# Kernel tuning notes

Measured on AMD Instinct MI355X. Metric: run time of the kernel, lower is better.

The kernel has to match this reference:

```python
import jax, jax.numpy as jnp
import numpy as np

GRID_MIN, GRID_MAX, GRID_SIZE = -4.0, 4.0, 12
BANDWIDTH = (GRID_MAX - GRID_MIN) / max(GRID_SIZE - 1, 1)  # 8/11


def setup_inputs() -> dict:
    key = jax.random.key(0)
    k1, k2, k3, k4 = jax.random.split(key, 4)
    B, I, O, G = 16384, 512, 512, GRID_SIZE
    x = jax.random.normal(k1, (B, I), dtype=jnp.float32)
    coeff = jax.random.normal(k2, (I, O, G), dtype=jnp.float32) * 0.05
    base_w = jax.random.normal(k3, (O, I), dtype=jnp.float32) * (1.0 / np.sqrt(I))
    base_b = jax.random.normal(k4, (O,), dtype=jnp.float32) * 0.01
    centers = jnp.linspace(GRID_MIN, GRID_MAX, G, dtype=jnp.float32)
    return {"x": x, "coeff": coeff, "base_w": base_w, "base_b": base_b, "centers": centers}


def reference(x, coeff, base_w, base_b, centers):
    # RBF basis: [B, I, G]
    diff = (x[..., None] - centers) / jnp.float32(BANDWIDTH)
    basis = jnp.exp(-0.5 * diff * diff)
    # spline contraction over in_dim and grid: [B, O]
    spline = jnp.einsum('big,iog->bo', basis, coeff)
    # residual base linear (torch Linear: x @ W^T + b)
    return spline + x @ base_w.T + base_b
```

## Files before the change

### kernel.cpp

```cpp
#include <hip/hip_runtime.h>
#include <hip/hip_bf16.h>


#define N_DIM 512
#define I_DIM 512
#define KTOT  6656
#define NSTEP 208

typedef short short8 __attribute__((ext_vector_type(8)));
typedef float f32x16 __attribute__((ext_vector_type(16)));
typedef unsigned int u32x4 __attribute__((ext_vector_type(4)));

#define CVTPK(dst, lo, hi) \
  asm("v_cvt_pk_bf16_f32 %0, %1, %2" : "=v"(dst) : "v"(lo), "v"(hi))

__device__ __forceinline__ unsigned short f2bf(float f) {
  union { float f; unsigned int u; } c; c.f = f;
  unsigned int r = (c.u + 0x7FFFu + ((c.u >> 16) & 1)) >> 16;
  return (unsigned short)r;
}

__global__ __launch_bounds__(256) void prep_w(const float* __restrict__ coeff,
                                              const float* __restrict__ base_w,
                                              unsigned short* __restrict__ Wb2) {
  int t = blockIdx.x * 256 + threadIdx.x;
  int e0 = (t & 1) * 4;
  int go = t >> 1;
  int o  = go & 511;
  int g  = go >> 9;
  int k4 = g * 8 + e0;
  int ic = k4 / 416;
  int rem = k4 - ic * 416;
  int slot = rem >> 5;
  int ii = rem & 31;
  int i = ic * 32 + ii;
  float v0, v1, v2, v3;
  if (slot == 0) {
    const float4 bw = *(const float4*)(base_w + (size_t)o * I_DIM + i);
    v0 = bw.x; v1 = bw.y; v2 = bw.z; v3 = bw.w;
  } else {
    int gg = slot - 1;
    const float* cp = coeff + (size_t)i * (N_DIM * 12) + o * 12 + gg;
    v0 = cp[0]; v1 = cp[6144]; v2 = cp[2 * 6144]; v3 = cp[3 * 6144];
  }
  ushort4 s;
  s.x = f2bf(v0); s.y = f2bf(v1); s.z = f2bf(v2); s.w = f2bf(v3);
  *(ushort4*)(Wb2 + (size_t)go * 8 + e0) = s;
}

__global__ __launch_bounds__(512, 2) void kan_gemm(const float* __restrict__ x,
                                                   const unsigned short* __restrict__ Wb2,
                                                   const float* __restrict__ bias,
                                                   float* __restrict__ out) {
  __shared__ unsigned short Asw[4 * 4 * 128 * 8];

  const int tid  = threadIdx.x;
  const int lane = tid & 63;
  const int wid  = tid >> 6;
  const int l31  = lane & 31, hl = lane >> 5;
  const bool isCons = (wid >= 4);

  const int bid = blockIdx.x;
  const int xcd = bid & 7, jj = bid >> 3;
  const int cb  = xcd >> 2;
  const int rb  = jj * 4 + (xcd & 3);
  const int M0  = rb * 128;
  const int N0  = cb * 256;

  const char* Wb = (const char*)Wb2;

  const int pid  = (wid & 3) * 64 + lane;
  const int prow = pid & 127;
  const int pkh  = pid >> 7;
  const float* xrow = x + (size_t)(M0 + prow) * I_DIM + pkh * 16;
  const int paoff0 = ((pkh * 2) * 128 + prow) * 16;
  const int paoff1 = ((pkh * 2 + 1) * 128 + prow) * 16;
  float bb[16], ff[16];
  int eslot = 0, echunk = 0;

  auto emitP = [&](char* pDst) {
    unsigned int w[8];
    if (eslot == 0) {
      const float* xp = xrow + echunk * 32;
      float4 p0 = *(const float4*)(xp);
      float4 p1 = *(const float4*)(xp + 4);
      float4 p2 = *(const float4*)(xp + 8);
      float4 p3 = *(const float4*)(xp + 12);
      float f[16] = {p0.x,p0.y,p0.z,p0.w, p1.x,p1.y,p1.z,p1.w,
                     p2.x,p2.y,p2.z,p2.w, p3.x,p3.y,p3.z,p3.w};
#pragma unroll
      for (int j = 0; j < 8; ++j) CVTPK(w[j], f[2*j], f[2*j+1]);
      *(u32x4*)(pDst + paoff0) = (u32x4){w[0], w[1], w[2], w[3]};
      *(u32x4*)(pDst + paoff1) = (u32x4){w[4], w[5], w[6], w[7]};
#pragma unroll
      for (int j = 0; j < 16; ++j) {
        float u = fmaf(f[j], 1.375f, 5.5f);
        bb[j] = exp2f(-0.72134752044448170f * u * u);
        ff[j] = exp2f(fmaf(u, 1.44269504088896340f, -0.72134752044448170f));
      }
    } else {
#pragma unroll
      for (int j = 0; j < 8; ++j) CVTPK(w[j], bb[2*j], bb[2*j+1]);
      *(u32x4*)(pDst + paoff0) = (u32x4){w[0], w[1], w[2], w[3]};
      *(u32x4*)(pDst + paoff1) = (u32x4){w[4], w[5], w[6], w[7]};
#pragma unroll
      for (int j = 0; j < 16; ++j) {
        bb[j] *= ff[j];
        ff[j] *= 0.36787944117144233f;
      }
    }
    if (eslot == 12) { eslot = 0; ++echunk; } else { ++eslot; }
  };

  const int cw = (wid & 3);
  int boff[2][2];
#pragma unroll
  for (int s = 0; s < 2; ++s)
#pragma unroll
    for (int fo = 0; fo < 2; ++fo)
      boff[s][fo] = (((s * 2 + hl) * 512) + N0 + cw * 64 + fo * 32 + l31) * 16;
  const int aBase = hl * 2048 + l31 * 16;

  f32x16 acc[4][2];
#pragma unroll
  for (int i = 0; i < 4; ++i)
#pragma unroll
    for (int j = 0; j < 2; ++j)
#pragma unroll
      for (int r = 0; r < 16; ++r) acc[i][j][r] = 0.f;

  short8 bvA[2][2], bvB[2][2];

  auto loadBinto = [&](short8 (&bv)[2][2], int tt) {
    const char* WbT = Wb + (size_t)tt * 32768;
#pragma unroll
    for (int s = 0; s < 2; ++s) {
      bv[s][0] = *(const short8*)(WbT + boff[s][0]);
      bv[s][1] = *(const short8*)(WbT + boff[s][1]);
    }
  };

  auto consStep = [&](int tt, short8 (&bv)[2][2], bool reload) {
    const char* pA = (const char*)Asw + ((tt & 3) << 13);
    short8 av[2][4];
#pragma unroll
    for (int s = 0; s < 2; ++s)
#pragma unroll
      for (int fb = 0; fb < 4; ++fb)
        av[s][fb] = *(const short8*)(pA + s * 4096 + fb * 512 + aBase);
#pragma unroll
    for (int s = 0; s < 2; ++s)
#pragma unroll
      for (int fb = 0; fb < 4; ++fb) {
        acc[fb][0] = __builtin_amdgcn_mfma_f32_32x32x16_bf16(av[s][fb], bv[s][0], acc[fb][0], 0, 0, 0);
        acc[fb][1] = __builtin_amdgcn_mfma_f32_32x32x16_bf16(av[s][fb], bv[s][1], acc[fb][1], 0, 0, 0);
      }
    if (reload) loadBinto(bv, tt + 2);
  };

  if (isCons) {
    loadBinto(bvA, 0);
    loadBinto(bvB, 1);
  } else {
    emitP((char*)Asw);
    emitP((char*)Asw + 8192);
  }
  asm volatile("s_waitcnt lgkmcnt(0)" ::: "memory");
  __builtin_amdgcn_s_barrier();

#pragma unroll 1
  for (int t = 0; t < 206; t += 2) {
    if (isCons) {
      consStep(t,     bvA, true);
      consStep(t + 1, bvB, true);
    } else {
      emitP((char*)Asw + (((t + 2) & 3) << 13));
      emitP((char*)Asw + (((t + 3) & 3) << 13));
    }
    asm volatile("s_waitcnt lgkmcnt(0)" ::: "memory");
    __builtin_amdgcn_s_barrier();
  }
  if (isCons) {
    consStep(206, bvA, false);
    consStep(207, bvB, false);

    float bvv[2];
#pragma unroll
    for (int fo = 0; fo < 2; ++fo) bvv[fo] = bias[N0 + cw * 64 + fo * 32 + l31];
    const int rbase = 4 * hl;
#pragma unroll
    for (int fb = 0; fb < 4; ++fb) {
#pragma unroll
      for (int fo = 0; fo < 2; ++fo) {
        const size_t cix = (size_t)(N0 + cw * 64 + fo * 32 + l31);
#pragma unroll
        for (int r = 0; r < 16; ++r) {
          int row = M0 + fb * 32 + (r & 3) + 8 * (r >> 2) + rbase;
          out[(size_t)row * N_DIM + cix] = acc[fb][fo][r] + bvv[fo];
        }
      }
    }
  }
}

extern "C" void kernel_launch(void* const* d_in, const int* in_sizes, int n_in,
                              void* d_out, int out_size, void* d_ws, size_t ws_size,
                              hipStream_t stream) {
  const float* x      = (const float*)d_in[0];
  const float* coeff  = (const float*)d_in[1];
  const float* base_w = (const float*)d_in[2];
  const float* base_b = (const float*)d_in[3];
  unsigned short* Wb2 = (unsigned short*)d_ws;

  prep_w<<<3328, 256, 0, stream>>>(coeff, base_w, Wb2);
  kan_gemm<<<256, 512, 0, stream>>>(x, Wb2, base_b, (float*)d_out);
}
```

Baseline: 132.2 us.

## Replace producer/consumer warp split with uniform waves on smaller 64x128 tiles

Removes the warp-specialised split in which four waves generated bf16 RBF basis tiles and four waves ran MFMAs. Now every wave of a 256-thread block both emits its slice of the A tile and issues MFMAs, interleaving the two within each step, with a barrier every two steps. The output tile per block shrinks from 128x256 to 64x128, giving 1024 blocks with four blocks per CU instead of 256 blocks with two. This should improve latency hiding and ALU/MFMA overlap across blocks. In exchange, each output tile is smaller, so x is re-read and the RBF basis recomputed more often, and B-tile reuse per load drops.

```diff
diff --git a/kernel.cpp b/kernel.cpp
--- a/kernel.cpp
+++ b/kernel.cpp
@@ -48,157 +48,131 @@
   *(ushort4*)(Wb2 + (size_t)go * 8 + e0) = s;
 }
 
-__global__ __launch_bounds__(512, 2) void kan_gemm(const float* __restrict__ x,
+__global__ __launch_bounds__(256, 4) void kan_gemm(const float* __restrict__ x,
                                                    const unsigned short* __restrict__ Wb2,
                                                    const float* __restrict__ bias,
                                                    float* __restrict__ out) {
-  __shared__ unsigned short Asw[4 * 4 * 128 * 8];
+  __shared__ unsigned short Asw[4 * 4 * 64 * 8];
 
   const int tid  = threadIdx.x;
   const int lane = tid & 63;
   const int wid  = tid >> 6;
+  const int wm   = wid >> 1, wn = wid & 1;
   const int l31  = lane & 31, hl = lane >> 5;
-  const bool isCons = (wid >= 4);
 
   const int bid = blockIdx.x;
-  const int xcd = bid & 7, jj = bid >> 3;
-  const int cb  = xcd >> 2;
-  const int rb  = jj * 4 + (xcd & 3);
-  const int M0  = rb * 128;
-  const int N0  = cb * 256;
+  const int xcd = bid & 7, j = bid >> 3;
+  const int cb  = xcd >> 1;
+  const int rb  = j * 2 + (xcd & 1);
+  const int M0  = rb * 64;
+  const int N0  = cb * 128;
+
+  const int arow = tid & 63;
+  const int kq   = tid >> 6;
+  const float* xrow = x + (size_t)(M0 + arow) * I_DIM + kq * 8;
+  const int aoff = (kq * 64 + arow) * 16;
 
   const char* Wb = (const char*)Wb2;
+  int boff[2][2];
+#pragma unroll
+  for (int ks = 0; ks < 2; ++ks)
+#pragma unroll
+    for (int fo = 0; fo < 2; ++fo)
+      boff[ks][fo] = (((ks * 2 + hl) * 512) + N0 + wn * 64 + fo * 32 + l31) * 16;
 
-  const int pid  = (wid & 3) * 64 + lane;
-  const int prow = pid & 127;
-  const int pkh  = pid >> 7;
-  const float* xrow = x + (size_t)(M0 + prow) * I_DIM + pkh * 16;
-  const int paoff0 = ((pkh * 2) * 128 + prow) * 16;
-  const int paoff1 = ((pkh * 2 + 1) * 128 + prow) * 16;
-  float bb[16], ff[16];
+  const int aBase = (wm * 32 + l31) * 16;
+
+  f32x16 acc[2];
+#pragma unroll
+  for (int fo = 0; fo < 2; ++fo)
+#pragma unroll
+    for (int r = 0; r < 16; ++r) acc[fo][r] = 0.f;
+
+  float bb[8], ff[8];
   int eslot = 0, echunk = 0;
 
-  auto emitP = [&](char* pDst) {
-    unsigned int w[8];
+  auto emitA = [&](char* pDst) {
+    unsigned int w[4];
     if (eslot == 0) {
       const float* xp = xrow + echunk * 32;
       float4 p0 = *(const float4*)(xp);
       float4 p1 = *(const float4*)(xp + 4);
-      float4 p2 = *(const float4*)(xp + 8);
-      float4 p3 = *(const float4*)(xp + 12);
-      float f[16] = {p0.x,p0.y,p0.z,p0.w, p1.x,p1.y,p1.z,p1.w,
-                     p2.x,p2.y,p2.z,p2.w, p3.x,p3.y,p3.z,p3.w};
+      float f[8] = {p0.x, p0.y, p0.z, p0.w, p1.x, p1.y, p1.z, p1.w};
 #pragma unroll
-      for (int j = 0; j < 8; ++j) CVTPK(w[j], f[2*j], f[2*j+1]);
-      *(u32x4*)(pDst + paoff0) = (u32x4){w[0], w[1], w[2], w[3]};
-      *(u32x4*)(pDst + paoff1) = (u32x4){w[4], w[5], w[6], w[7]};
+      for (int j2 = 0; j2 < 4; ++j2) CVTPK(w[j2], f[2*j2], f[2*j2+1]);
+      *(u32x4*)(pDst + aoff) = (u32x4){w[0], w[1], w[2], w[3]};
 #pragma unroll
-      for (int j = 0; j < 16; ++j) {
-        float u = fmaf(f[j], 1.375f, 5.5f);
-        bb[j] = exp2f(-0.72134752044448170f * u * u);
-        ff[j] = exp2f(fmaf(u, 1.44269504088896340f, -0.72134752044448170f));
+      for (int j2 = 0; j2 < 8; ++j2) {
+        float u = fmaf(f[j2], 1.375f, 5.5f);
+        bb[j2] = exp2f(-0.72134752044448170f * u * u);
+        ff[j2] = exp2f(fmaf(u, 1.44269504088896340f, -0.72134752044448170f));
       }
     } else {
 #pragma unroll
-      for (int j = 0; j < 8; ++j) CVTPK(w[j], bb[2*j], bb[2*j+1]);
-      *(u32x4*)(pDst + paoff0) = (u32x4){w[0], w[1], w[2], w[3]};
-      *(u32x4*)(pDst + paoff1) = (u32x4){w[4], w[5], w[6], w[7]};
+      for (int j2 = 0; j2 < 4; ++j2) CVTPK(w[j2], bb[2*j2], bb[2*j2+1]);
+      *(u32x4*)(pDst + aoff) = (u32x4){w[0], w[1], w[2], w[3]};
 #pragma unroll
-      for (int j = 0; j < 16; ++j) {
-        bb[j] *= ff[j];
-        ff[j] *= 0.36787944117144233f;
+      for (int j2 = 0; j2 < 8; ++j2) {
+        bb[j2] *= ff[j2];
+        ff[j2] *= 0.36787944117144233f;
       }
     }
     if (eslot == 12) { eslot = 0; ++echunk; } else { ++eslot; }
   };
 
-  const int cw = (wid & 3);
-  int boff[2][2];
-#pragma unroll
-  for (int s = 0; s < 2; ++s)
-#pragma unroll
-    for (int fo = 0; fo < 2; ++fo)
-      boff[s][fo] = (((s * 2 + hl) * 512) + N0 + cw * 64 + fo * 32 + l31) * 16;
-  const int aBase = hl * 2048 + l31 * 16;
-
-  f32x16 acc[4][2];
-#pragma unroll
-  for (int i = 0; i < 4; ++i)
-#pragma unroll
-    for (int j = 0; j < 2; ++j)
-#pragma unroll
-      for (int r = 0; r < 16; ++r) acc[i][j][r] = 0.f;
-
   short8 bvA[2][2], bvB[2][2];
 
-  auto loadBinto = [&](short8 (&bv)[2][2], int tt) {
+  auto loadB = [&](short8 (&bv)[2][2], int tt) {
     const char* WbT = Wb + (size_t)tt * 32768;
 #pragma unroll
-    for (int s = 0; s < 2; ++s) {
-      bv[s][0] = *(const short8*)(WbT + boff[s][0]);
-      bv[s][1] = *(const short8*)(WbT + boff[s][1]);
+    for (int ks = 0; ks < 2; ++ks) {
+      bv[ks][0] = *(const short8*)(WbT + boff[ks][0]);
+      bv[ks][1] = *(const short8*)(WbT + boff[ks][1]);
     }
   };
 
-  auto consStep = [&](int tt, short8 (&bv)[2][2], bool reload) {
-    const char* pA = (const char*)Asw + ((tt & 3) << 13);
-    short8 av[2][4];
-#pragma unroll
-    for (int s = 0; s < 2; ++s)
-#pragma unroll
-      for (int fb = 0; fb < 4; ++fb)
-        av[s][fb] = *(const short8*)(pA + s * 4096 + fb * 512 + aBase);
-#pragma unroll
-    for (int s = 0; s < 2; ++s)
-#pragma unroll
-      for (int fb = 0; fb < 4; ++fb) {
-        acc[fb][0] = __builtin_amdgcn_mfma_f32_32x32x16_bf16(av[s][fb], bv[s][0], acc[fb][0], 0, 0, 0);
-        acc[fb][1] = __builtin_amdgcn_mfma_f32_32x32x16_bf16(av[s][fb], bv[s][1], acc[fb][1], 0, 0, 0);
-      }
-    if (reload) loadBinto(bv, tt + 2);
+  auto stepBody = [&](int tt, int rdOff, int emOff,
+                      short8 (&bvC)[2][2], short8 (&bvN)[2][2]) {
+    if (tt < NSTEP - 1) loadB(bvN, tt + 1);
+    const char* pA = (const char*)Asw + rdOff;
+    short8 av0 = *(const short8*)(pA + (0 * 2 + hl) * 1024 + aBase);
+    short8 av1 = *(const short8*)(pA + (1 * 2 + hl) * 1024 + aBase);
+    if (tt < NSTEP - 2) emitA((char*)Asw + emOff);
+    acc[0] = __builtin_amdgcn_mfma_f32_32x32x16_bf16(av0, bvC[0][0], acc[0], 0, 0, 0);
+    acc[1] = __builtin_amdgcn_mfma_f32_32x32x16_bf16(av0, bvC[0][1], acc[1], 0, 0, 0);
+    acc[0] = __builtin_amdgcn_mfma_f32_32x32x16_bf16(av1, bvC[1][0], acc[0], 0, 0, 0);
+    acc[1] = __builtin_amdgcn_mfma_f32_32x32x16_bf16(av1, bvC[1][1], acc[1], 0, 0, 0);
   };
 
-  if (isCons) {
-    loadBinto(bvA, 0);
-    loadBinto(bvB, 1);
-  } else {
-    emitP((char*)Asw);
-    emitP((char*)Asw + 8192);
-  }
+  emitA((char*)Asw);
+  emitA((char*)Asw + 4096);
+  loadB(bvA, 0);
   asm volatile("s_waitcnt lgkmcnt(0)" ::: "memory");
   __builtin_amdgcn_s_barrier();
 
 #pragma unroll 1
-  for (int t = 0; t < 206; t += 2) {
-    if (isCons) {
-      consStep(t,     bvA, true);
-      consStep(t + 1, bvB, true);
-    } else {
-      emitP((char*)Asw + (((t + 2) & 3) << 13));
-      emitP((char*)Asw + (((t + 3) & 3) << 13));
-    }
+  for (int t = 0; t < NSTEP; t += 4) {
+    stepBody(t,     0,     8192,  bvA, bvB);
+    stepBody(t + 1, 4096,  12288, bvB, bvA);
+    asm volatile("s_waitcnt lgkmcnt(0)" ::: "memory");
+    __builtin_amdgcn_s_barrier();
+    stepBody(t + 2, 8192,  0,     bvA, bvB);
+    stepBody(t + 3, 12288, 4096,  bvB, bvA);
     asm volatile("s_waitcnt lgkmcnt(0)" ::: "memory");
     __builtin_amdgcn_s_barrier();
   }
-  if (isCons) {
-    consStep(206, bvA, false);
-    consStep(207, bvB, false);
 
-    float bvv[2];
+  float bvv[2];
 #pragma unroll
-    for (int fo = 0; fo < 2; ++fo) bvv[fo] = bias[N0 + cw * 64 + fo * 32 + l31];
-    const int rbase = 4 * hl;
+  for (int fo = 0; fo < 2; ++fo) bvv[fo] = bias[N0 + wn * 64 + fo * 32 + l31];
+  const int rbase = 4 * hl;
 #pragma unroll
-    for (int fb = 0; fb < 4; ++fb) {
+  for (int fo = 0; fo < 2; ++fo) {
+    const size_t cix = (size_t)(N0 + wn * 64 + fo * 32 + l31);
 #pragma unroll
-      for (int fo = 0; fo < 2; ++fo) {
-        const size_t cix = (size_t)(N0 + cw * 64 + fo * 32 + l31);
-#pragma unroll
-        for (int r = 0; r < 16; ++r) {
-          int row = M0 + fb * 32 + (r & 3) + 8 * (r >> 2) + rbase;
-          out[(size_t)row * N_DIM + cix] = acc[fb][fo][r] + bvv[fo];
-        }
-      }
+    for (int r = 0; r < 16; ++r) {
+      int row = M0 + wm * 32 + (r & 3) + 8 * (r >> 2) + rbase;
+      out[(size_t)row * N_DIM + cix] = acc[fo][r] + bvv[fo];
     }
   }
 }
@@ -213,5 +187,5 @@
   unsigned short* Wb2 = (unsigned short*)d_ws;
 
   prep_w<<<3328, 256, 0, stream>>>(coeff, base_w, Wb2);
-  kan_gemm<<<256, 512, 0, stream>>>(x, Wb2, base_b, (float*)d_out);
+  kan_gemm<<<1024, 256, 0, stream>>>(x, Wb2, base_b, (float*)d_out);
 }
```

Result: slower. 211.1 us (+59.7%).
